# Optimization experiments

Hardware: AMD Instinct MI355X
Metric: run time of the kernel (lower is better)

## Reference

```python
import jax, jax.numpy as jnp
import numpy as np

N_HEAD = 16

def setup_inputs() -> dict:
    key = jax.random.key(0)
    k1, k2, k3 = jax.random.split(key, 3)
    B, S, D = 2, 2048, 1024
    x = jax.random.normal(k1, (B, S, D), dtype=jnp.float32)
    w_attn = jax.random.normal(k2, (D, 3 * D), dtype=jnp.float32) * 0.02
    b_attn = jnp.zeros((3 * D,), dtype=jnp.float32)
    w_proj = jax.random.normal(k3, (D, D), dtype=jnp.float32) * 0.02
    b_proj = jnp.zeros((D,), dtype=jnp.float32)
    return {"x": x, "w_attn": w_attn, "b_attn": b_attn, "w_proj": w_proj, "b_proj": b_proj}

def reference(x, w_attn, b_attn, w_proj, b_proj):
    B, S, D = x.shape
    H = N_HEAD
    dh = D // H
    # c_attn: fused QKV projection
    qkv = jnp.einsum('bsd,df->bsf', x, w_attn) + b_attn  # [B,S,3D]
    q, k, v = jnp.split(qkv, 3, axis=-1)
    # split heads -> [B,H,S,dh]
    def heads(t):
        return t.reshape(B, S, H, dh).transpose(0, 2, 1, 3)
    q, k, v = heads(q), heads(k), heads(v)
    # NOTE: causal bias buffer is unused in the original forward -> non-causal attention
    scores = jnp.einsum('bhqd,bhkd->bhqk', q, k) / jnp.sqrt(jnp.float32(dh))
    probs = jax.nn.softmax(scores, axis=-1)
    out = jnp.einsum('bhqk,bhkd->bhqd', probs, v)
    # merge heads
    out = out.transpose(0, 2, 1, 3).reshape(B, S, D)
    # c_proj
    return jnp.einsum('bsd,de->bse', out, w_proj) + b_proj
```

## Files before the change

### kernel.cpp

```cpp
#include <hip/hip_runtime.h>

typedef __attribute__((ext_vector_type(8))) short short8;
typedef __attribute__((ext_vector_type(4))) float f32x4;
typedef unsigned short u16;
typedef unsigned int   u32;

#define S_  2048
#define D_  1024
#define H_  16
#define DH_ 64
#define M_  4096
#define K_  1024
#define N3_ 3072

__device__ __forceinline__ u16 f2bf(float f) {
    u32 u = __float_as_uint(f);
    u32 r = u + 0x7FFFu + ((u >> 16) & 1u);
    return (u16)(r >> 16);
}

__device__ __forceinline__ void gload_lds16(const void* g, void* l) {
    __builtin_amdgcn_global_load_lds(
        (const __attribute__((address_space(1))) u32*)g,
        (__attribute__((address_space(3))) u32*)l, 16, 0, 0);
}

__global__ __launch_bounds__(256) void convert_f32_bf16(
    const float* __restrict__ in, u16* __restrict__ out, int n4)
{
    int i = blockIdx.x * 256 + threadIdx.x;
    const int stride = gridDim.x * 256;
    for (; i < n4; i += stride) {
        float4 v = ((const float4*)in)[i];
        ushort4 o;
        o.x = f2bf(v.x); o.y = f2bf(v.y); o.z = f2bf(v.z); o.w = f2bf(v.w);
        ((ushort4*)out)[i] = o;
    }
}

__global__ __launch_bounds__(256) void transpose_f32_bf16(
    const float* __restrict__ in, u16* __restrict__ out, int rows, int cols)
{
    __shared__ float tile[32][33];
    const int tx = threadIdx.x & 31;
    const int ty = threadIdx.x >> 5;
    #pragma unroll
    for (int i = 0; i < 4; ++i) {
        int r = blockIdx.y * 32 + ty + i * 8;
        int c = blockIdx.x * 32 + tx;
        tile[ty + i * 8][tx] = in[(size_t)r * cols + c];
    }
    __syncthreads();
    #pragma unroll
    for (int i = 0; i < 4; ++i) {
        int orow = blockIdx.x * 32 + ty + i * 8;
        int ocol = blockIdx.y * 32 + tx;
        out[(size_t)orow * rows + ocol] = f2bf(tile[tx][ty + i * 8]);
    }
}

template <int EPI>
__global__ __launch_bounds__(256) void mfma_gemm(
    const u16* __restrict__ A, const u16* __restrict__ Bt,
    const float* __restrict__ bias,
    u16* __restrict__ qd, u16* __restrict__ kd, u16* __restrict__ vd,
    float* __restrict__ outp)
{
    __shared__ u16 As[128 * 32];
    __shared__ u16 Bs[128 * 32];

    const int t  = threadIdx.x;
    const int wv = t >> 6;
    const int ln = t & 63;
    const int wr = wv >> 1, wc = wv & 1;
    const int r0 = blockIdx.y * 128;
    const int c0 = blockIdx.x * 128;
    const int li = ln & 15, lq = ln >> 4;

    f32x4 acc[4][4];
    #pragma unroll
    for (int m = 0; m < 4; ++m)
        #pragma unroll
        for (int n = 0; n < 4; ++n) acc[m][n] = (f32x4){0.f, 0.f, 0.f, 0.f};

    for (int k0 = 0; k0 < K_; k0 += 32) {
        __syncthreads();
        #pragma unroll
        for (int qq = 0; qq < 2; ++qq) {
            const int slot = wv * 128 + qq * 64 + ln;
            const int row  = slot >> 2;
            const int col  = (slot & 3) * 8;
            gload_lds16(A  + (size_t)(r0 + row) * K_ + k0 + col,
                        &As[(size_t)(wv * 128 + qq * 64) * 8]);
            gload_lds16(Bt + (size_t)(c0 + row) * K_ + k0 + col,
                        &Bs[(size_t)(wv * 128 + qq * 64) * 8]);
        }
        __syncthreads();

        short8 af[4], bfr[4];
        const int qk = lq * 8;
        #pragma unroll
        for (int m = 0; m < 4; ++m)
            af[m] = *(const short8*)&As[(wr * 64 + m * 16 + li) * 32 + qk];
        #pragma unroll
        for (int n = 0; n < 4; ++n)
            bfr[n] = *(const short8*)&Bs[(wc * 64 + n * 16 + li) * 32 + qk];
        #pragma unroll
        for (int m = 0; m < 4; ++m)
            #pragma unroll
            for (int n = 0; n < 4; ++n)
                acc[m][n] = __builtin_amdgcn_mfma_f32_16x16x32_bf16(
                    af[m], bfr[n], acc[m][n], 0, 0, 0);
    }

    if (EPI == 0) {
        #pragma unroll
        for (int n = 0; n < 4; ++n) {
            const int gcol  = c0 + wc * 64 + n * 16 + li;
            const int which = gcol >> 10;
            const int rem   = gcol & 1023;
            const int h     = rem >> 6;
            const int dh    = rem & 63;
            const float scl = (which == 0) ? 0.125f : 1.0f;
            const float bb  = bias[gcol];
            #pragma unroll
            for (int m = 0; m < 4; ++m)
                #pragma unroll
                for (int r = 0; r < 4; ++r) {
                    const int grow = r0 + wr * 64 + m * 16 + lq * 4 + r;
                    const int b = grow >> 11, s = grow & (S_ - 1);
                    const u16 val = f2bf((acc[m][n][r] + bb) * scl);
                    if (which == 2) {
                        vd[((size_t)(b * H_ + h) * DH_ + dh) * S_ + s] = val;
                    } else {
                        u16* dst = (which == 0) ? qd : kd;
                        dst[((size_t)(b * H_ + h) * S_ + s) * DH_ + dh] = val;
                    }
                }
        }
    } else {
        #pragma unroll
        for (int n = 0; n < 4; ++n) {
            const int gcol = c0 + wc * 64 + n * 16 + li;
            const float bb = bias[gcol];
            #pragma unroll
            for (int m = 0; m < 4; ++m)
                #pragma unroll
                for (int r = 0; r < 4; ++r) {
                    const int grow = r0 + wr * 64 + m * 16 + lq * 4 + r;
                    outp[(size_t)grow * D_ + gcol] = acc[m][n][r] + bb;
                }
        }
    }
}

__global__ __launch_bounds__(256, 4) void attn_mfma(
    const u16* __restrict__ qws, const u16* __restrict__ kws,
    const u16* __restrict__ vtws, u16* __restrict__ ao)
{
    __shared__ u16 Ks[64 * 64];
    __shared__ u16 Vt[64 * 64];
    __shared__ u16 Ps[64 * 64];

    const int t  = threadIdx.x;
    const int wv = t >> 6, ln = t & 63;
    const int li = ln & 15, lq = ln >> 4;
    const int bh = blockIdx.y;
    const int q0 = blockIdx.x * 64;

    const u16* Kp  = kws  + (size_t)bh * S_ * DH_;
    const u16* Vtp = vtws + (size_t)bh * DH_ * S_;

    short8 aq[2];
    {
        const u16* Qp = qws + ((size_t)bh * S_ + q0 + wv * 16 + li) * DH_ + lq * 8;
        aq[0] = *(const short8*)(Qp);
        aq[1] = *(const short8*)(Qp + 32);
    }

    f32x4 o[4];
    #pragma unroll
    for (int n = 0; n < 4; ++n) o[n] = (f32x4){0.f, 0.f, 0.f, 0.f};
    float mrow[4] = {-3e38f, -3e38f, -3e38f, -3e38f};
    float lrow[4] = {0.f, 0.f, 0.f, 0.f};

    for (int kt = 0; kt < S_ / 64; ++kt) {
        const int k0 = kt * 64;
        __syncthreads();
        #pragma unroll
        for (int i = 0; i < 2; ++i) {
            const int s   = t + i * 256;
            const int row = s >> 3;
            const int c16 = s & 7;
            const int off = (row * 128 + c16 * 16) ^ ((row & 7) << 4);
            *(short8*)((char*)Ks + off) =
                *(const short8*)(Kp + (size_t)(k0 + row) * DH_ + c16 * 8);
            *(short8*)((char*)Vt + off) =
                *(const short8*)(Vtp + (size_t)row * S_ + k0 + c16 * 8);
        }
        __syncthreads();

        f32x4 sacc[4];
        #pragma unroll
        for (int j = 0; j < 4; ++j) sacc[j] = (f32x4){0.f, 0.f, 0.f, 0.f};
        __builtin_amdgcn_s_setprio(1);
        #pragma unroll
        for (int ks = 0; ks < 2; ++ks) {
            #pragma unroll
            for (int j = 0; j < 4; ++j) {
                const int rrow = j * 16 + li;
                const int roff = (rrow * 128 + ks * 64 + lq * 16) ^ ((li & 7) << 4);
                short8 bk = *(const short8*)((char*)Ks + roff);
                sacc[j] = __builtin_amdgcn_mfma_f32_16x16x32_bf16(aq[ks], bk, sacc[j], 0, 0, 0);
            }
        }
        __builtin_amdgcn_s_setprio(0);

        #pragma unroll
        for (int r = 0; r < 4; ++r) {
            float mx = fmaxf(fmaxf(sacc[0][r], sacc[1][r]), fmaxf(sacc[2][r], sacc[3][r]));
            mx = fmaxf(mx, __shfl_xor(mx, 1));
            mx = fmaxf(mx, __shfl_xor(mx, 2));
            mx = fmaxf(mx, __shfl_xor(mx, 4));
            mx = fmaxf(mx, __shfl_xor(mx, 8));
            const float mnew = fmaxf(mrow[r], mx);
            const float p0 = __expf(sacc[0][r] - mnew);
            const float p1 = __expf(sacc[1][r] - mnew);
            const float p2 = __expf(sacc[2][r] - mnew);
            const float p3 = __expf(sacc[3][r] - mnew);
            float rs = p0 + p1 + p2 + p3;
            rs += __shfl_xor(rs, 1);
            rs += __shfl_xor(rs, 2);
            rs += __shfl_xor(rs, 4);
            rs += __shfl_xor(rs, 8);
            const float scl = __expf(mrow[r] - mnew);
            lrow[r] = lrow[r] * scl + rs;
            mrow[r] = mnew;
            const int prow = wv * 16 + lq * 4 + r;
            const int pbase = prow * 128;
            const int psw   = (prow & 7) << 4;
            *(u16*)((char*)Ps + ((pbase + (     li) * 2) ^ psw)) = f2bf(p0);
            *(u16*)((char*)Ps + ((pbase + (16 + li) * 2) ^ psw)) = f2bf(p1);
            *(u16*)((char*)Ps + ((pbase + (32 + li) * 2) ^ psw)) = f2bf(p2);
            *(u16*)((char*)Ps + ((pbase + (48 + li) * 2) ^ psw)) = f2bf(p3);
            #pragma unroll
            for (int n = 0; n < 4; ++n) o[n][r] *= scl;
        }

        __builtin_amdgcn_s_setprio(1);
        #pragma unroll
        for (int ks = 0; ks < 2; ++ks) {
            const int arow = wv * 16 + li;
            const int aoff = (arow * 128 + ks * 64 + lq * 16) ^ ((li & 7) << 4);
            short8 ap = *(const short8*)((char*)Ps + aoff);
            #pragma unroll
            for (int n = 0; n < 4; ++n) {
                const int vrow = n * 16 + li;
                const int voff = (vrow * 128 + ks * 64 + lq * 16) ^ ((li & 7) << 4);
                short8 bv = *(const short8*)((char*)Vt + voff);
                o[n] = __builtin_amdgcn_mfma_f32_16x16x32_bf16(ap, bv, o[n], 0, 0, 0);
            }
        }
        __builtin_amdgcn_s_setprio(0);
    }

    const int b = bh >> 4, h = bh & 15;
    #pragma unroll
    for (int r = 0; r < 4; ++r) {
        const float inv = 1.0f / lrow[r];
        const int s = q0 + wv * 16 + lq * 4 + r;
        #pragma unroll
        for (int n = 0; n < 4; ++n) {
            const int col = h * 64 + n * 16 + li;
            ao[((size_t)b * S_ + s) * D_ + col] = f2bf(o[n][r] * inv);
        }
    }
}

extern "C" void kernel_launch(void* const* d_in, const int* in_sizes, int n_in,
                              void* d_out, int out_size, void* d_ws, size_t ws_size,
                              hipStream_t stream)
{
    const float* x      = (const float*)d_in[0];
    const float* w_attn = (const float*)d_in[1];
    const float* b_attn = (const float*)d_in[2];
    const float* w_proj = (const float*)d_in[3];
    const float* b_proj = (const float*)d_in[4];
    float* out = (float*)d_out;

    char* ws = (char*)d_ws;
    u16* x_bf = (u16*)(ws);
    u16* wat  = (u16*)(ws + 8388608);
    u16* wpj  = (u16*)(ws + 14680064);
    u16* qws  = (u16*)(ws + 16777216);
    u16* kws  = (u16*)(ws + 25165824);
    u16* vtws = (u16*)(ws + 33554432);
    u16* ao   = (u16*)(ws + 41943040);

    convert_f32_bf16<<<1024, 256, 0, stream>>>(x, x_bf, M_ * K_ / 4);
    transpose_f32_bf16<<<dim3(N3_ / 32, K_ / 32), 256, 0, stream>>>(w_attn, wat, K_, N3_);
    transpose_f32_bf16<<<dim3(D_ / 32, K_ / 32), 256, 0, stream>>>(w_proj, wpj, K_, D_);

    mfma_gemm<0><<<dim3(N3_ / 128, M_ / 128), 256, 0, stream>>>(
        x_bf, wat, b_attn, qws, kws, vtws, nullptr);

    attn_mfma<<<dim3(S_ / 64, 32), 256, 0, stream>>>(qws, kws, vtws, ao);

    mfma_gemm<1><<<dim3(D_ / 128, M_ / 128), 256, 0, stream>>>(
        ao, wpj, b_proj, nullptr, nullptr, nullptr, out);
}
```

Before: 253.4 us.

## Double-buffer attention K/V, lazy softmax rescale, exp2, XCD-aware block remapping

Attention now prefetches the next K/V tile into registers and double-buffers it in LDS, so global loads overlap compute and one barrier per iteration is removed. Q is pre-scaled by log2(e)/sqrt(dh) so exp2 can replace exp, and the running-max rescale of the accumulator is skipped unless the max grows by more than a threshold. Probabilities and V outputs are stored as packed vector writes instead of scalar u16 stores. Both GEMMs and attention use 1D grids remapped so neighbouring tiles and heads land on the same XCD for L2 locality. These changes add register pressure and rely on the lazy-rescale threshold keeping the exponentials in range.

After: 265.1 us. 1.05x slower.

```diff
diff --git a/kernel.cpp b/kernel.cpp
--- a/kernel.cpp
+++ b/kernel.cpp
@@ -1,4 +1,5 @@
 #include <hip/hip_runtime.h>
+#include <hip/hip_bf16.h>
 
 typedef __attribute__((ext_vector_type(8))) short short8;
 typedef __attribute__((ext_vector_type(4))) float f32x4;
@@ -13,10 +14,20 @@
 #define K_  1024
 #define N3_ 3072
 
+#define QSCL 0.18033688011112042f
+
 __device__ __forceinline__ u16 f2bf(float f) {
     u32 u = __float_as_uint(f);
     u32 r = u + 0x7FFFu + ((u >> 16) & 1u);
     return (u16)(r >> 16);
+}
+
+__device__ __forceinline__ float fast_exp2(float x) {
+#if __has_builtin(__builtin_amdgcn_exp2f)
+    return __builtin_amdgcn_exp2f(x);
+#else
+    return __expf(x * 0.6931471805599453f);
+#endif
 }
 
 __device__ __forceinline__ void gload_lds16(const void* g, void* l) {
@@ -64,7 +75,7 @@
     const u16* __restrict__ A, const u16* __restrict__ Bt,
     const float* __restrict__ bias,
     u16* __restrict__ qd, u16* __restrict__ kd, u16* __restrict__ vd,
-    float* __restrict__ outp)
+    float* __restrict__ outp, int nx)
 {
     __shared__ u16 As[128 * 32];
     __shared__ u16 Bs[128 * 32];
@@ -73,8 +84,10 @@
     const int wv = t >> 6;
     const int ln = t & 63;
     const int wr = wv >> 1, wc = wv & 1;
-    const int r0 = blockIdx.y * 128;
-    const int c0 = blockIdx.x * 128;
+    const int cpx  = gridDim.x >> 3;
+    const int wgid = (blockIdx.x & 7) * cpx + (blockIdx.x >> 3);
+    const int r0 = (wgid / nx) * 128;
+    const int c0 = (wgid % nx) * 128;
     const int li = ln & 15, lq = ln >> 4;
 
     f32x4 acc[4][4];
@@ -121,22 +134,32 @@
             const int rem   = gcol & 1023;
             const int h     = rem >> 6;
             const int dh    = rem & 63;
-            const float scl = (which == 0) ? 0.125f : 1.0f;
             const float bb  = bias[gcol];
-            #pragma unroll
-            for (int m = 0; m < 4; ++m)
+            if (which == 2) {
                 #pragma unroll
-                for (int r = 0; r < 4; ++r) {
-                    const int grow = r0 + wr * 64 + m * 16 + lq * 4 + r;
-                    const int b = grow >> 11, s = grow & (S_ - 1);
-                    const u16 val = f2bf((acc[m][n][r] + bb) * scl);
-                    if (which == 2) {
-                        vd[((size_t)(b * H_ + h) * DH_ + dh) * S_ + s] = val;
-                    } else {
-                        u16* dst = (which == 0) ? qd : kd;
-                        dst[((size_t)(b * H_ + h) * S_ + s) * DH_ + dh] = val;
+                for (int m = 0; m < 4; ++m) {
+                    const int grow0 = r0 + wr * 64 + m * 16 + lq * 4;
+                    const int b = grow0 >> 11, sb = grow0 & (S_ - 1);
+                    uint2 pk;
+                    pk.x = (u32)f2bf(acc[m][n][0] + bb) |
+                           ((u32)f2bf(acc[m][n][1] + bb) << 16);
+                    pk.y = (u32)f2bf(acc[m][n][2] + bb) |
+                           ((u32)f2bf(acc[m][n][3] + bb) << 16);
+                    *(uint2*)(vd + ((size_t)(b * H_ + h) * DH_ + dh) * S_ + sb) = pk;
+                }
+            } else {
+                const float scl = (which == 0) ? QSCL : 1.0f;
+                u16* dst = (which == 0) ? qd : kd;
+                #pragma unroll
+                for (int m = 0; m < 4; ++m)
+                    #pragma unroll
+                    for (int r = 0; r < 4; ++r) {
+                        const int grow = r0 + wr * 64 + m * 16 + lq * 4 + r;
+                        const int b = grow >> 11, s = grow & (S_ - 1);
+                        dst[((size_t)(b * H_ + h) * S_ + s) * DH_ + dh] =
+                            f2bf((acc[m][n][r] + bb) * scl);
                     }
-                }
+            }
         }
     } else {
         #pragma unroll
@@ -158,15 +181,19 @@
     const u16* __restrict__ qws, const u16* __restrict__ kws,
     const u16* __restrict__ vtws, u16* __restrict__ ao)
 {
-    __shared__ u16 Ks[64 * 64];
-    __shared__ u16 Vt[64 * 64];
+    __shared__ u16 Ks[2][64 * 64];
+    __shared__ u16 Vt[2][64 * 64];
     __shared__ u16 Ps[64 * 64];
 
     const int t  = threadIdx.x;
     const int wv = t >> 6, ln = t & 63;
     const int li = ln & 15, lq = ln >> 4;
-    const int bh = blockIdx.y;
-    const int q0 = blockIdx.x * 64;
+
+    const int f    = blockIdx.x;
+    const int xcd  = f & 7;
+    const int slot = f >> 3;
+    const int bh   = xcd * 4 + (slot >> 5);
+    const int q0   = (slot & 31) * 64;
 
     const u16* Kp  = kws  + (size_t)bh * S_ * DH_;
     const u16* Vtp = vtws + (size_t)bh * DH_ * S_;
@@ -178,6 +205,17 @@
         aq[1] = *(const short8*)(Qp + 32);
     }
 
+    const int s0 = t, s1 = t + 256;
+    const int row0 = s0 >> 3, c0e = (s0 & 7) * 8;
+    const int row1 = s1 >> 3, c1e = (s1 & 7) * 8;
+    const int off0 = (row0 * 128 + c0e * 2) ^ ((row0 & 7) << 4);
+    const int off1 = (row1 * 128 + c1e * 2) ^ ((row1 & 7) << 4);
+
+    short8 ldK0 = *(const short8*)(Kp  + (size_t)row0 * DH_ + c0e);
+    short8 ldK1 = *(const short8*)(Kp  + (size_t)row1 * DH_ + c1e);
+    short8 ldV0 = *(const short8*)(Vtp + (size_t)row0 * S_  + c0e);
+    short8 ldV1 = *(const short8*)(Vtp + (size_t)row1 * S_  + c1e);
+
     f32x4 o[4];
     #pragma unroll
     for (int n = 0; n < 4; ++n) o[n] = (f32x4){0.f, 0.f, 0.f, 0.f};
@@ -185,18 +223,18 @@
     float lrow[4] = {0.f, 0.f, 0.f, 0.f};
 
     for (int kt = 0; kt < S_ / 64; ++kt) {
-        const int k0 = kt * 64;
-        __syncthreads();
-        #pragma unroll
-        for (int i = 0; i < 2; ++i) {
-            const int s   = t + i * 256;
-            const int row = s >> 3;
-            const int c16 = s & 7;
-            const int off = (row * 128 + c16 * 16) ^ ((row & 7) << 4);
-            *(short8*)((char*)Ks + off) =
-                *(const short8*)(Kp + (size_t)(k0 + row) * DH_ + c16 * 8);
-            *(short8*)((char*)Vt + off) =
-                *(const short8*)(Vtp + (size_t)row * S_ + k0 + c16 * 8);
+        u16* Kb = Ks[kt & 1];
+        u16* Vb = Vt[kt & 1];
+        *(short8*)((char*)Kb + off0) = ldK0;
+        *(short8*)((char*)Kb + off1) = ldK1;
+        *(short8*)((char*)Vb + off0) = ldV0;
+        *(short8*)((char*)Vb + off1) = ldV1;
+        if (kt + 1 < S_ / 64) {
+            const int k0n = (kt + 1) * 64;
+            ldK0 = *(const short8*)(Kp  + (size_t)(k0n + row0) * DH_ + c0e);
+            ldK1 = *(const short8*)(Kp  + (size_t)(k0n + row1) * DH_ + c1e);
+            ldV0 = *(const short8*)(Vtp + (size_t)row0 * S_ + k0n + c0e);
+            ldV1 = *(const short8*)(Vtp + (size_t)row1 * S_ + k0n + c1e);
         }
         __syncthreads();
 
@@ -208,14 +246,15 @@
         for (int ks = 0; ks < 2; ++ks) {
             #pragma unroll
             for (int j = 0; j < 4; ++j) {
-                const int rrow = j * 16 + li;
-                const int roff = (rrow * 128 + ks * 64 + lq * 16) ^ ((li & 7) << 4);
-                short8 bk = *(const short8*)((char*)Ks + roff);
+                const int rrow = li * 4 + j;
+                const int roff = (rrow * 128 + ks * 64 + lq * 16) ^ ((rrow & 7) << 4);
+                short8 bk = *(const short8*)((char*)Kb + roff);
                 sacc[j] = __builtin_amdgcn_mfma_f32_16x16x32_bf16(aq[ks], bk, sacc[j], 0, 0, 0);
             }
         }
         __builtin_amdgcn_s_setprio(0);
 
+        float rmx[4];
         #pragma unroll
         for (int r = 0; r < 4; ++r) {
             float mx = fmaxf(fmaxf(sacc[0][r], sacc[1][r]), fmaxf(sacc[2][r], sacc[3][r]));
@@ -223,28 +262,41 @@
             mx = fmaxf(mx, __shfl_xor(mx, 2));
             mx = fmaxf(mx, __shfl_xor(mx, 4));
             mx = fmaxf(mx, __shfl_xor(mx, 8));
-            const float mnew = fmaxf(mrow[r], mx);
-            const float p0 = __expf(sacc[0][r] - mnew);
-            const float p1 = __expf(sacc[1][r] - mnew);
-            const float p2 = __expf(sacc[2][r] - mnew);
-            const float p3 = __expf(sacc[3][r] - mnew);
+            rmx[r] = mx;
+        }
+        const bool grow = (rmx[0] > mrow[0] + 8.f) | (rmx[1] > mrow[1] + 8.f) |
+                          (rmx[2] > mrow[2] + 8.f) | (rmx[3] > mrow[3] + 8.f);
+        if (__any(grow)) {
+            #pragma unroll
+            for (int r = 0; r < 4; ++r) {
+                const float mnew = fmaxf(mrow[r], rmx[r]);
+                const float scl  = fast_exp2(mrow[r] - mnew);
+                lrow[r] *= scl;
+                #pragma unroll
+                for (int n = 0; n < 4; ++n) o[n][r] *= scl;
+                mrow[r] = mnew;
+            }
+        }
+        #pragma unroll
+        for (int r = 0; r < 4; ++r) {
+            const float p0 = fast_exp2(sacc[0][r] - mrow[r]);
+            const float p1 = fast_exp2(sacc[1][r] - mrow[r]);
+            const float p2 = fast_exp2(sacc[2][r] - mrow[r]);
+            const float p3 = fast_exp2(sacc[3][r] - mrow[r]);
             float rs = p0 + p1 + p2 + p3;
             rs += __shfl_xor(rs, 1);
             rs += __shfl_xor(rs, 2);
             rs += __shfl_xor(rs, 4);
             rs += __shfl_xor(rs, 8);
-            const float scl = __expf(mrow[r] - mnew);
-            lrow[r] = lrow[r] * scl + rs;
-            mrow[r] = mnew;
+            lrow[r] += rs;
+            __hip_bfloat162 h01 = __float22bfloat162_rn(make_float2(p0, p1));
+            __hip_bfloat162 h23 = __float22bfloat162_rn(make_float2(p2, p3));
+            uint2 pk;
+            pk.x = *(const u32*)&h01;
+            pk.y = *(const u32*)&h23;
             const int prow = wv * 16 + lq * 4 + r;
-            const int pbase = prow * 128;
-            const int psw   = (prow & 7) << 4;
-            *(u16*)((char*)Ps + ((pbase + (     li) * 2) ^ psw)) = f2bf(p0);
-            *(u16*)((char*)Ps + ((pbase + (16 + li) * 2) ^ psw)) = f2bf(p1);
-            *(u16*)((char*)Ps + ((pbase + (32 + li) * 2) ^ psw)) = f2bf(p2);
-            *(u16*)((char*)Ps + ((pbase + (48 + li) * 2) ^ psw)) = f2bf(p3);
-            #pragma unroll
-            for (int n = 0; n < 4; ++n) o[n][r] *= scl;
+            const int pb   = (prow * 128 + li * 8) ^ ((prow & 7) << 4);
+            *(uint2*)((char*)Ps + pb) = pk;
         }
 
         __builtin_amdgcn_s_setprio(1);
@@ -257,7 +309,7 @@
             for (int n = 0; n < 4; ++n) {
                 const int vrow = n * 16 + li;
                 const int voff = (vrow * 128 + ks * 64 + lq * 16) ^ ((li & 7) << 4);
-                short8 bv = *(const short8*)((char*)Vt + voff);
+                short8 bv = *(const short8*)((char*)Vb + voff);
                 o[n] = __builtin_amdgcn_mfma_f32_16x16x32_bf16(ap, bv, o[n], 0, 0, 0);
             }
         }
@@ -301,11 +353,11 @@
     transpose_f32_bf16<<<dim3(N3_ / 32, K_ / 32), 256, 0, stream>>>(w_attn, wat, K_, N3_);
     transpose_f32_bf16<<<dim3(D_ / 32, K_ / 32), 256, 0, stream>>>(w_proj, wpj, K_, D_);
 
-    mfma_gemm<0><<<dim3(N3_ / 128, M_ / 128), 256, 0, stream>>>(
-        x_bf, wat, b_attn, qws, kws, vtws, nullptr);
-
-    attn_mfma<<<dim3(S_ / 64, 32), 256, 0, stream>>>(qws, kws, vtws, ao);
-
-    mfma_gemm<1><<<dim3(D_ / 128, M_ / 128), 256, 0, stream>>>(
-        ao, wpj, b_proj, nullptr, nullptr, nullptr, out);
-}
+    mfma_gemm<0><<<dim3((N3_ / 128) * (M_ / 128)), 256, 0, stream>>>(
+        x_bf, wat, b_attn, qws, kws, vtws, nullptr, N3_ / 128);
+
+    attn_mfma<<<dim3(1024), 256, 0, stream>>>(qws, kws, vtws, ao);
+
+    mfma_gemm<1><<<dim3((D_ / 128) * (M_ / 128)), 256, 0, stream>>>(
+        ao, wpj, b_proj, nullptr, nullptr, nullptr, out, D_ / 128);
+}
```
